# Optimization experiments

Measured on AMD Instinct MI355X. Metric: run time of the kernel, lower is better.

## Reference

```python
import jax, jax.numpy as jnp
import numpy as np

B, C, H, W = 32, 128, 32, 32
E, K, D, HID = 16, 2, 128, 512  # nbExperts, topK, nbIn=nbOut, hidden=4*max(nbIn,nbOut)


def setup_inputs() -> dict:
    key = jax.random.key(0)
    ks = jax.random.split(key, 6)
    init = lambda k, shape, fan: (jax.random.normal(k, shape, jnp.float32) / np.sqrt(fan)).astype(jnp.float32)
    return {
        "x": jax.random.normal(ks[0], (B, C, H, W), jnp.float32),
        "gate_w": init(ks[1], (D, E), D),
        "gate_b": jnp.zeros((E,), jnp.float32),
        "noise_w": init(ks[2], (D, E), D),
        "noise_b": jnp.zeros((E,), jnp.float32),
        "w1": init(ks[3], (E, D, HID), D),
        "b1": jnp.zeros((E, HID), jnp.float32),
        "w2": init(ks[4], (E, HID, D), HID),
        "b2": jnp.zeros((E, D), jnp.float32),
        "top_k": K,
    }


def reference(x, gate_w, gate_b, noise_w, noise_b, w1, b1, w2, b2, top_k):
    b, c, h, w = x.shape
    xt = x.transpose(0, 2, 3, 1).reshape(-1, c)  # [T, D] tokens (fromCNN path)
    T = xt.shape[0]

    # --- GatingWithNoise: gate(x) + randn * softplus(noise(x)) ---
    logits = xt @ gate_w + gate_b                      # [T, E]
    noise_sd = jax.nn.softplus(xt @ noise_w + noise_b)  # [T, E]
    noise = jax.random.normal(jax.random.key(42), logits.shape, logits.dtype)
    logits = logits + noise * noise_sd

    # --- top-k, softmax over k, scatter to dense [T, E] gate matrix ---
    top_vals, top_idx = jax.lax.top_k(logits, top_k)   # [T, K]
    probs = jax.nn.softmax(top_vals, axis=1)           # [T, K]
    gates = jnp.zeros((T, E), x.dtype).at[jnp.arange(T)[:, None], top_idx].set(probs)

    # --- dense path: run every expert, weighted combine ---
    hdn = jax.nn.relu(jnp.einsum('td,edh->teh', xt, w1) + b1)  # [T, E, HID]
    eo = jnp.einsum('teh,ehd->ted', hdn, w2) + b2              # [T, E, D]
    out = jnp.einsum('te,ted->td', gates, eo)                  # [T, D]

    out = out.reshape(b, h, w, c).transpose(0, 3, 1, 2)        # back to NCHW
    gates = gates.reshape(b, h, w, E)
    return out, gates
```

## Files before the change

### kernel.cpp

```cpp
#include <hip/hip_runtime.h>
#include <stdint.h>

#define NB       32
#define NC       128
#define NHW      1024
#define NT       32768
#define NE       16
#define NHID     512

typedef __attribute__((ext_vector_type(8))) short short8v;
typedef __attribute__((ext_vector_type(4))) float f32x4;

__device__ __forceinline__ unsigned short f2bf(float f) {
    uint32_t u = __float_as_uint(f);
    uint32_t r = u + 0x7fffu + ((u >> 16) & 1u);
    return (unsigned short)(r >> 16);
}
__device__ __forceinline__ float bf2f(unsigned short u) {
    return __uint_as_float(((uint32_t)u) << 16);
}

__device__ __forceinline__ void gll16(const void* g, void* l) {
    __builtin_amdgcn_global_load_lds(
        (const __attribute__((address_space(1))) uint32_t*)g,
        (__attribute__((address_space(3))) uint32_t*)l, 16, 0, 0);
}

#define WAIT_VMLGKM() asm volatile("s_waitcnt vmcnt(0) lgkmcnt(0)" ::: "memory")
#define WAIT_LGKM()   asm volatile("s_waitcnt lgkmcnt(0)" ::: "memory")
#define SBAR()        { asm volatile("" ::: "memory"); __builtin_amdgcn_s_barrier(); asm volatile("" ::: "memory"); }

__device__ __forceinline__ uint32_t rotl32(uint32_t x, uint32_t d) {
    return (x << d) | (x >> (32u - d));
}

__device__ __forceinline__ void threefry2x32_20(uint32_t k0, uint32_t k1,
                                                uint32_t& x0, uint32_t& x1) {
    const uint32_t ks0 = k0, ks1 = k1, ks2 = k0 ^ k1 ^ 0x1BD11BDAu;
    x0 += ks0; x1 += ks1;
#define TFR(r) { x0 += x1; x1 = rotl32(x1, r); x1 ^= x0; }
    TFR(13u) TFR(15u) TFR(26u) TFR(6u)
    x0 += ks1; x1 += ks2 + 1u;
    TFR(17u) TFR(29u) TFR(16u) TFR(24u)
    x0 += ks2; x1 += ks0 + 2u;
    TFR(13u) TFR(15u) TFR(26u) TFR(6u)
    x0 += ks0; x1 += ks1 + 3u;
    TFR(17u) TFR(29u) TFR(16u) TFR(24u)
    x0 += ks1; x1 += ks2 + 4u;
    TFR(13u) TFR(15u) TFR(26u) TFR(6u)
    x0 += ks2; x1 += ks0 + 5u;
#undef TFR
}

__device__ __forceinline__ float erfinv_xla_f32(float x) {
    float w = -log1pf(-x * x);
    float p;
    if (w < 5.0f) {
        w = w - 2.5f;
        p = 2.81022636e-08f;
        p = fmaf(p, w, 3.43273939e-07f);
        p = fmaf(p, w, -3.5233877e-06f);
        p = fmaf(p, w, -4.39150654e-06f);
        p = fmaf(p, w, 0.00021858087f);
        p = fmaf(p, w, -0.00125372503f);
        p = fmaf(p, w, -0.00417768164f);
        p = fmaf(p, w, 0.246640727f);
        p = fmaf(p, w, 1.50140941f);
    } else {
        w = sqrtf(w) - 3.0f;
        p = -0.000200214257f;
        p = fmaf(p, w, 0.000100950558f);
        p = fmaf(p, w, 0.00134934322f);
        p = fmaf(p, w, -0.00367342844f);
        p = fmaf(p, w, 0.00573950773f);
        p = fmaf(p, w, -0.0076224613f);
        p = fmaf(p, w, 0.00943887047f);
        p = fmaf(p, w, 1.00167406f);
        p = fmaf(p, w, 2.83297682f);
    }
    return p * x;
}

__device__ __forceinline__ float jax_noise_elem(uint32_t i) {
    uint32_t x0 = 0u, x1 = i;
    threefry2x32_20(0u, 42u, x0, x1);
    uint32_t bits = x0 ^ x1;
    float f = __uint_as_float(0x3f800000u | (bits >> 9)) - 1.0f;
    const float lo = -0.99999994f;
    float u = f * 2.0f + lo;
    u = fmaxf(lo, u);
    return 1.41421354f * erfinv_xla_f32(u);
}

__global__ __launch_bounds__(256) void moe_gate_kernel(
    const float* __restrict__ x,
    const float* __restrict__ gate_w, const float* __restrict__ gate_b,
    const float* __restrict__ noise_w, const float* __restrict__ noise_b,
    float* __restrict__ gates_out,
    int*   __restrict__ top_idx,
    float* __restrict__ top_prob,
    int*   __restrict__ rank,
    int*   __restrict__ cnt,
    unsigned short* __restrict__ xtb,
    int do_new)
{
    __shared__ float lw[32 * 160];
    __shared__ int   lcnt[16];
    __shared__ int   lbase[16];

    const int tid = threadIdx.x;
    const int tl  = tid >> 2;
    const int q   = tid & 3;
    const int t   = blockIdx.x * 64 + tl;
    const int b   = t >> 10, hw = t & 1023;

    if (tid < 16) lcnt[tid] = 0;

    for (int idx = tid; idx < 4096; idx += 256) {
        int ci = idx >> 7;
        int r  = idx & 127;
        int qq = r >> 5, e = r & 31;
        int c  = qq * 32 + ci;
        float v = (e < 16) ? gate_w[c * 16 + e] : noise_w[c * 16 + (e - 16)];
        lw[ci * 160 + qq * 40 + e] = v;
    }
    __syncthreads();

    float acc[32];
    #pragma unroll
    for (int e = 0; e < 32; ++e) acc[e] = 0.f;

    unsigned short xh[32];
    const float* xq = x + (size_t)b * (NC * NHW) + (size_t)(q * 32) * NHW + hw;
    const float* wq = lw + q * 40;
    #pragma unroll 4
    for (int ci = 0; ci < 32; ++ci) {
        float xv = xq[(size_t)ci << 10];
        xh[ci] = f2bf(xv);
        const f32x4* wr = (const f32x4*)(wq + ci * 160);
        #pragma unroll
        for (int j = 0; j < 8; ++j) {
            f32x4 w4 = wr[j];
            #pragma unroll
            for (int k = 0; k < 4; ++k)
                acc[j * 4 + k] = fmaf(xv, w4[k], acc[j * 4 + k]);
        }
    }

    if (do_new) {
        #pragma unroll
        for (int j = 0; j < 4; ++j) {
            short8v v;
            #pragma unroll
            for (int k = 0; k < 8; ++k) v[k] = (short)xh[j * 8 + k];
            *(short8v*)(xtb + (size_t)t * 128 + q * 32 + j * 8) = v;
        }
    }

    #pragma unroll
    for (int e = 0; e < 32; ++e) {
        acc[e] += __shfl_xor(acc[e], 1);
        acc[e] += __shfl_xor(acc[e], 2);
    }

    float lg[4];
    #pragma unroll
    for (int j = 0; j < 4; ++j) {
        int e = q * 4 + j;
        float g  = acc[e] + gate_b[e];
        float an = acc[16 + e] + noise_b[e];
        float sd = fmaxf(an, 0.f) + log1pf(expf(-fabsf(an)));
        float nz = jax_noise_elem((uint32_t)t * 16u + (uint32_t)e);
        lg[j] = fmaf(nz, sd, g);
    }

    float v1 = lg[0], v2 = -INFINITY;
    int   i1 = q * 4, i2 = 0x7fffffff;
    #pragma unroll
    for (int j = 1; j < 4; ++j) {
        float v = lg[j]; int e = q * 4 + j;
        if (v > v1) { v2 = v1; i2 = i1; v1 = v; i1 = e; }
        else if (v > v2) { v2 = v; i2 = e; }
    }
    #pragma unroll
    for (int m = 1; m <= 2; m <<= 1) {
        float pv1 = __shfl_xor(v1, m), pv2 = __shfl_xor(v2, m);
        int   pi1 = __shfl_xor(i1, m), pi2 = __shfl_xor(i2, m);
        bool pBest = (pv1 > v1) || (pv1 == v1 && pi1 < i1);
        float c2v; int c2i;
        if (pBest) { c2v = v1;  c2i = i1;  v1 = pv1; i1 = pi1;
                     if (!((c2v > pv2) || (c2v == pv2 && c2i < pi2))) { c2v = pv2; c2i = pi2; }
        } else     { c2v = pv1; c2i = pi1;
                     if (!((c2v > v2)  || (c2v == v2  && c2i < i2)))  { c2v = v2;  c2i = i2;  }
        }
        v2 = c2v; i2 = c2i;
    }

    float qq = expf(v2 - v1);
    float s  = 1.0f + qq;
    float p1 = 1.0f / s;
    float p2 = qq / s;

    f32x4 g4;
    #pragma unroll
    for (int j = 0; j < 4; ++j) {
        int e = q * 4 + j;
        g4[j] = (e == i1) ? p1 : ((e == i2) ? p2 : 0.f);
    }
    *(f32x4*)(gates_out + (size_t)t * 16 + q * 4) = g4;

    int r1 = 0, r2 = 0;
    if (q == 0) {
        top_idx[t * 2 + 0] = i1;  top_idx[t * 2 + 1] = i2;
        top_prob[t * 2 + 0] = p1; top_prob[t * 2 + 1] = p2;
        if (do_new) {
            r1 = atomicAdd(&lcnt[i1], 1);
            r2 = atomicAdd(&lcnt[i2], 1);
        }
    }
    if (do_new) {
        __syncthreads();
        if (tid < 16) lbase[tid] = atomicAdd(&cnt[tid], lcnt[tid]);
        __syncthreads();
        if (q == 0) {
            rank[t * 2 + 0] = lbase[i1] + r1;
            rank[t * 2 + 1] = lbase[i2] + r2;
        }
    }
}

__global__ __launch_bounds__(256) void transpose_convert_kernel(
    const float* __restrict__ src, unsigned short* __restrict__ dst, int R, int C)
{
    __shared__ float ts[64][65];
    const int nr = R >> 6, ncc = C >> 6;
    const int blk = blockIdx.x;
    const int e = blk / (nr * ncc);
    const int rem = blk % (nr * ncc);
    const int rt = rem / ncc, ct = rem % ncc;
    const float* S = src + (size_t)e * R * C + (size_t)(rt * 64) * C + ct * 64;
    unsigned short* D = dst + (size_t)e * R * C + (size_t)(ct * 64) * R + rt * 64;
    const int tid = threadIdx.x;
    #pragma unroll
    for (int i = 0; i < 16; ++i) {
        int lin = i * 256 + tid;
        int r = lin >> 6, c = lin & 63;
        ts[r][c] = S[(size_t)r * C + c];
    }
    __syncthreads();
    #pragma unroll
    for (int i = 0; i < 16; ++i) {
        int lin = i * 256 + tid;
        int c = lin >> 6, r = lin & 63;
        D[(size_t)c * R + r] = f2bf(ts[r][c]);
    }
}

__global__ __launch_bounds__(256) void scan_kernel(
    const int* __restrict__ cnt,
    int* __restrict__ poff, int* __restrict__ blk2e,
    int* __restrict__ blk2chunk, int* __restrict__ total_chunks,
    int* __restrict__ pair_tok)
{
    __shared__ int snch[16];
    __shared__ int scum[17];
    __shared__ int spoff[16];
    const int tid = threadIdx.x;
    if (tid < 16) snch[tid] = (cnt[tid] + 127) >> 7;
    __syncthreads();
    if (tid == 0) {
        int cc = 0, off = 0;
        for (int e = 0; e < 16; ++e) {
            scum[e] = cc; spoff[e] = off;
            cc += snch[e]; off += snch[e] << 7;
        }
        scum[16] = cc;
        *total_chunks = cc;
    }
    __syncthreads();
    const int tot = scum[16];
    for (int idx = tid; idx < tot; idx += 256) {
        int e = 0;
        #pragma unroll
        for (int k = 0; k < 15; ++k)
            if (idx >= scum[k + 1]) e = k + 1;
        blk2e[idx] = e;
        blk2chunk[idx] = idx - scum[e];
    }
    if (tid < 16) poff[tid] = spoff[tid];
    for (int e = 0; e < 16; ++e) {
        int start = spoff[e] + cnt[e];
        int end   = spoff[e] + (snch[e] << 7);
        for (int i = start + tid; i < end; i += 256)
            pair_tok[i] = -1;
    }
}

__global__ __launch_bounds__(256) void scatter_kernel(
    const int* __restrict__ top_idx, const int* __restrict__ rank,
    const int* __restrict__ poff, int* __restrict__ pair_tok,
    int* __restrict__ slot_of)
{
    int i = blockIdx.x * 256 + threadIdx.x;
    int t = i >> 1;
    int e = top_idx[i];
    int slot = poff[e] + rank[i];
    pair_tok[slot] = t;
    slot_of[i] = slot;
}

__device__ __forceinline__ void stage_w1(const unsigned short* w1e, short* W1s,
                                         int hcn, int wid, int lane) {
    #pragma unroll
    for (int k2 = 0; k2 < 2; ++k2) {
        int i2 = wid * 2 + k2;
        int r2 = i2 * 4 + (lane >> 4);
        int s2 = lane & 15;
        gll16(w1e + (size_t)(hcn + r2) * 128 + ((s2 ^ (r2 & 15)) * 8),
              W1s + i2 * 512);
    }
}
__device__ __forceinline__ void stage_w2(const unsigned short* w2e, short* W2s,
                                         int hcn, int wid, int lane) {
    #pragma unroll
    for (int k2 = 0; k2 < 2; ++k2) {
        int i2 = wid * 2 + k2;
        int r2 = i2 * 8 + (lane >> 3);
        int s2 = lane & 7;
        gll16(w2e + (size_t)r2 * 512 + hcn + ((s2 ^ (r2 & 7)) * 8),
              W2s + i2 * 512);
    }
}

__global__ __launch_bounds__(512, 4) void moe_mfma_kernel(
    const unsigned short* __restrict__ xtb,
    const int* __restrict__ pair_tok, const int* __restrict__ blk2e,
    const int* __restrict__ blk2chunk, const int* __restrict__ poff,
    const int* __restrict__ total_chunks,
    const unsigned short* __restrict__ w1bt,
    const float* __restrict__ b1,
    const unsigned short* __restrict__ w2bt,
    const float* __restrict__ b2,
    unsigned short* __restrict__ pair_y)
{
    __shared__ short Xs[128 * 128];
    __shared__ short Hs[128 * 64];
    __shared__ short W1s[64 * 128];
    __shared__ short W2s[128 * 64];

    const int blk = blockIdx.x;
    if (blk >= *total_chunks) return;
    const int e  = blk2e[blk];
    const int p0 = poff[e] + (blk2chunk[blk] << 7);
    const int tid  = threadIdx.x;
    const int lane = tid & 63;
    const int wid  = tid >> 6;
    const int wm   = wid >> 1;
    const int wn   = wid & 1;
    const int l16  = lane & 15;
    const int lg   = lane >> 4;

    const unsigned short* w1e = w1bt + (size_t)e * 512 * 128;
    const unsigned short* w2e = w2bt + (size_t)e * 128 * 512;

    stage_w1(w1e, W1s, 0, wid, lane);
    stage_w2(w2e, W2s, 0, wid, lane);

    #pragma unroll
    for (int i = 0; i < 4; ++i) {
        int lin = i * 512 + tid;
        int row = lin >> 4, kc = lin & 15;
        int tok = pair_tok[p0 + row];
        short8v v = {};
        if (tok >= 0)
            v = *(const short8v*)(xtb + (size_t)tok * 128 + kc * 8);
        *(short8v*)(Xs + row * 128 + ((kc ^ (row & 15)) * 8)) = v;
    }

    f32x4 yacc[2][4];
    #pragma unroll
    for (int mi = 0; mi < 2; ++mi)
        #pragma unroll
        for (int ni = 0; ni < 4; ++ni)
            yacc[mi][ni] = (f32x4){0.f, 0.f, 0.f, 0.f};

    const int rowA0 = wm * 32 + l16, rowA1 = rowA0 + 16;

    for (int c = 0; c < 8; ++c) {
        WAIT_VMLGKM(); SBAR();

        f32x4 hacc[2][2];
        #pragma unroll
        for (int mi = 0; mi < 2; ++mi)
            #pragma unroll
            for (int ni = 0; ni < 2; ++ni)
                hacc[mi][ni] = (f32x4){0.f, 0.f, 0.f, 0.f};

        #pragma unroll
        for (int kk = 0; kk < 4; ++kk) {
            int slot = kk * 4 + lg;
            short8v a0 = *(const short8v*)(Xs + rowA0 * 128 + ((slot ^ (rowA0 & 15)) * 8));
            short8v a1 = *(const short8v*)(Xs + rowA1 * 128 + ((slot ^ (rowA1 & 15)) * 8));
            #pragma unroll
            for (int ni = 0; ni < 2; ++ni) {
                int hr = wn * 32 + ni * 16 + l16;
                short8v bfr = *(const short8v*)(W1s + hr * 128 + ((slot ^ (hr & 15)) * 8));
                hacc[0][ni] = __builtin_amdgcn_mfma_f32_16x16x32_bf16(a0, bfr, hacc[0][ni], 0, 0, 0);
                hacc[1][ni] = __builtin_amdgcn_mfma_f32_16x16x32_bf16(a1, bfr, hacc[1][ni], 0, 0, 0);
            }
        }
        #pragma unroll
        for (int ni = 0; ni < 2; ++ni) {
            int col = wn * 32 + ni * 16 + l16;
            float b1v = b1[e * 512 + (c << 6) + col];
            #pragma unroll
            for (int mi = 0; mi < 2; ++mi) {
                #pragma unroll
                for (int r = 0; r < 4; ++r) {
                    int m = wm * 32 + mi * 16 + lg * 4 + r;
                    float v = fmaxf(hacc[mi][ni][r] + b1v, 0.f);
                    Hs[m * 64 + (((col >> 3) ^ (m & 7)) << 3) + (col & 7)] = (short)f2bf(v);
                }
            }
        }
        WAIT_LGKM(); SBAR();

        if (c < 7) stage_w1(w1e, W1s, (c + 1) << 6, wid, lane);

        #pragma unroll
        for (int kk = 0; kk < 2; ++kk) {
            int slot = kk * 4 + lg;
            short8v a0 = *(const short8v*)(Hs + rowA0 * 64 + ((slot ^ (rowA0 & 7)) * 8));
            short8v a1 = *(const short8v*)(Hs + rowA1 * 64 + ((slot ^ (rowA1 & 7)) * 8));
            #pragma unroll
            for (int ni = 0; ni < 4; ++ni) {
                int dr = wn * 64 + ni * 16 + l16;
                short8v bfr = *(const short8v*)(W2s + dr * 64 + ((slot ^ (dr & 7)) * 8));
                yacc[0][ni] = __builtin_amdgcn_mfma_f32_16x16x32_bf16(a0, bfr, yacc[0][ni], 0, 0, 0);
                yacc[1][ni] = __builtin_amdgcn_mfma_f32_16x16x32_bf16(a1, bfr, yacc[1][ni], 0, 0, 0);
            }
        }
        WAIT_LGKM(); SBAR();

        if (c < 7) stage_w2(w2e, W2s, (c + 1) << 6, wid, lane);
    }

    #pragma unroll
    for (int ni = 0; ni < 4; ++ni) {
        int d = wn * 64 + ni * 16 + l16;
        float b2v = b2[e * 128 + d];
        #pragma unroll
        for (int mi = 0; mi < 2; ++mi) {
            #pragma unroll
            for (int r = 0; r < 4; ++r) {
                int m = wm * 32 + mi * 16 + lg * 4 + r;
                pair_y[(size_t)(p0 + m) * 128 + d] = f2bf(yacc[mi][ni][r] + b2v);
            }
        }
    }
}

__global__ __launch_bounds__(256) void combine_kernel(
    const unsigned short* __restrict__ pair_y, const int* __restrict__ slot_of,
    const float* __restrict__ top_prob, float* __restrict__ out)
{
    __shared__ float ob[64][129];
    const int blk = blockIdx.x;
    const int b = blk >> 4;
    const int hw0 = (blk & 15) << 6;
    const int tid = threadIdx.x;
    #pragma unroll
    for (int i = 0; i < 4; ++i) {
        int lin = i * 256 + tid;
        int tl = lin >> 4, dg = lin & 15;
        int t = b * 1024 + hw0 + tl;
        int s0 = slot_of[t * 2], s1 = slot_of[t * 2 + 1];
        float p0 = top_prob[t * 2], p1 = top_prob[t * 2 + 1];
        short8v y0 = *(const short8v*)(pair_y + (size_t)s0 * 128 + dg * 8);
        short8v y1 = *(const short8v*)(pair_y + (size_t)s1 * 128 + dg * 8);
        #pragma unroll
        for (int j = 0; j < 8; ++j)
            ob[tl][dg * 8 + j] = p0 * bf2f((unsigned short)y0[j]) + p1 * bf2f((unsigned short)y1[j]);
    }
    __syncthreads();
    #pragma unroll
    for (int i = 0; i < 32; ++i) {
        int lin = i * 256 + tid;
        int d = lin >> 6, hwl = lin & 63;
        out[((size_t)b * 128 + d) * 1024 + hw0 + hwl] = ob[hwl][d];
    }
}

__global__ __launch_bounds__(256) void moe_expert_kernel(
    const float* __restrict__ x,
    const int* __restrict__ top_idx, const float* __restrict__ top_prob,
    const float* __restrict__ w1, const float* __restrict__ b1,
    const float* __restrict__ w2, const float* __restrict__ b2,
    float* __restrict__ out)
{
    __shared__ float xsB[128];
    __shared__ float hb[512];

    const int tid = threadIdx.x;
    const int t = blockIdx.x;
    const int b = t >> 10, hw = t & 1023;

    if (tid < 128)
        xsB[tid] = x[((size_t)b * 128 + tid) * NHW + hw];
    __syncthreads();

    float oacc = 0.f;
    #pragma unroll
    for (int k = 0; k < 2; ++k) {
        const int e = top_idx[t * 2 + k];
        const float pw = top_prob[t * 2 + k];
        const float* W1 = w1 + (size_t)e * (128 * 512);
        float a0 = 0.f, a1 = 0.f;
        for (int d = 0; d < 128; ++d) {
            float xv = xsB[d];
            a0 = fmaf(xv, W1[d * 512 + tid], a0);
            a1 = fmaf(xv, W1[d * 512 + tid + 256], a1);
        }
        hb[tid]       = fmaxf(a0 + b1[e * 512 + tid], 0.f);
        hb[tid + 256] = fmaxf(a1 + b1[e * 512 + tid + 256], 0.f);
        __syncthreads();
        if (tid < 128) {
            const float* W2 = w2 + (size_t)e * (512 * 128);
            float a = 0.f;
            for (int h = 0; h < 512; ++h)
                a = fmaf(hb[h], W2[h * 128 + tid], a);
            oacc = fmaf(pw, a + b2[e * 128 + tid], oacc);
        }
        __syncthreads();
    }
    if (tid < 128)
        out[((size_t)b * 128 + tid) * NHW + hw] = oacc;
}

extern "C" void kernel_launch(void* const* d_in, const int* in_sizes, int n_in,
                              void* d_out, int out_size, void* d_ws, size_t ws_size,
                              hipStream_t stream) {
    const float* x       = (const float*)d_in[0];
    const float* gate_w  = (const float*)d_in[1];
    const float* gate_b  = (const float*)d_in[2];
    const float* noise_w = (const float*)d_in[3];
    const float* noise_b = (const float*)d_in[4];
    const float* w1      = (const float*)d_in[5];
    const float* b1      = (const float*)d_in[6];
    const float* w2      = (const float*)d_in[7];
    const float* b2      = (const float*)d_in[8];

    float* out   = (float*)d_out;
    float* gates = out + (size_t)NB * NC * NHW;

    const size_t OFF_CNT    = 0;
    const size_t OFF_POFF   = 1024;
    const size_t OFF_TOTAL  = 2048;
    const size_t OFF_B2E    = 4096;
    const size_t OFF_B2C    = 8192;
    const size_t OFF_TIDX   = 12288;
    const size_t OFF_RANK   = OFF_TIDX + (size_t)NT * 2 * 4;
    const size_t OFF_SLOT   = OFF_RANK + (size_t)NT * 2 * 4;
    const size_t OFF_PROB   = OFF_SLOT + (size_t)NT * 2 * 4;
    const size_t OFF_XTB    = OFF_PROB + (size_t)NT * 2 * 4;
    const size_t OFF_W1BT   = OFF_XTB + (size_t)NT * 128 * 2;
    const size_t OFF_W2BT   = OFF_W1BT + (size_t)NE * 512 * 128 * 2;
    const size_t OFF_PTOK   = OFF_W2BT + (size_t)NE * 128 * 512 * 2;
    const size_t NPAIR_PAD  = 67584;
    const size_t OFF_PAIRY  = OFF_PTOK + NPAIR_PAD * 4;
    const size_t NEED       = OFF_PAIRY + NPAIR_PAD * 128 * 2;

    char* ws = (char*)d_ws;
    int*   cnt      = (int*)(ws + OFF_CNT);
    int*   poff     = (int*)(ws + OFF_POFF);
    int*   total_ch = (int*)(ws + OFF_TOTAL);
    int*   blk2e    = (int*)(ws + OFF_B2E);
    int*   blk2c    = (int*)(ws + OFF_B2C);
    int*   top_idx  = (int*)(ws + OFF_TIDX);
    int*   rank     = (int*)(ws + OFF_RANK);
    int*   slot_of  = (int*)(ws + OFF_SLOT);
    float* top_prob = (float*)(ws + OFF_PROB);
    unsigned short* xtb    = (unsigned short*)(ws + OFF_XTB);
    unsigned short* w1bt   = (unsigned short*)(ws + OFF_W1BT);
    unsigned short* w2bt   = (unsigned short*)(ws + OFF_W2BT);
    int*   pair_tok = (int*)(ws + OFF_PTOK);
    unsigned short* pair_y = (unsigned short*)(ws + OFF_PAIRY);

    const int use_new = (ws_size >= NEED) ? 1 : 0;

    if (use_new)
        hipMemsetAsync(cnt, 0, 16 * sizeof(int), stream);

    moe_gate_kernel<<<NT / 64, 256, 0, stream>>>(
        x, gate_w, gate_b, noise_w, noise_b,
        gates, top_idx, top_prob, rank, cnt, xtb, use_new);

    if (use_new) {
        transpose_convert_kernel<<<NE * 2 * 8, 256, 0, stream>>>(w1, w1bt, 128, 512);
        transpose_convert_kernel<<<NE * 8 * 2, 256, 0, stream>>>(w2, w2bt, 512, 128);
        scan_kernel<<<1, 256, 0, stream>>>(cnt, poff, blk2e, blk2c, total_ch, pair_tok);
        scatter_kernel<<<NT * 2 / 256, 256, 0, stream>>>(top_idx, rank, poff, pair_tok, slot_of);
        moe_mfma_kernel<<<528, 512, 0, stream>>>(
            xtb, pair_tok, blk2e, blk2c, poff, total_ch,
            w1bt, b1, w2bt, b2, pair_y);
        combine_kernel<<<512, 256, 0, stream>>>(pair_y, slot_of, top_prob, out);
    } else {
        moe_expert_kernel<<<NT, 256, 0, stream>>>(
            x, top_idx, top_prob, w1, b1, w2, b2, out);
    }
}
```

Baseline: 96.68 us.

## Replace global atomic expert counters with per-block counts and merge transpose launches

The gate kernel now writes per-block expert counts and local ranks instead of doing global atomicAdd on shared counters. The scan kernel computes per-block base offsets with a two-level prefix sum, and scatter uses those bases. This removes the memset launch and the global atomics, and makes slot assignment deterministic. The two weight transpose launches are also merged into one, cutting launch overhead. In exchange the single-block scan kernel does more serial work.

Measured after the change: 95.64 us. No clear change (-1.1%).

```diff
diff --git a/kernel.cpp b/kernel.cpp
--- a/kernel.cpp
+++ b/kernel.cpp
@@ -7,6 +7,7 @@
 #define NT       32768
 #define NE       16
 #define NHID     512
+#define NGBLK    512
 
 typedef __attribute__((ext_vector_type(8))) short short8v;
 typedef __attribute__((ext_vector_type(4))) float f32x4;
@@ -100,13 +101,12 @@
     int*   __restrict__ top_idx,
     float* __restrict__ top_prob,
     int*   __restrict__ rank,
-    int*   __restrict__ cnt,
+    int*   __restrict__ bcnt,
     unsigned short* __restrict__ xtb,
     int do_new)
 {
     __shared__ float lw[32 * 160];
     __shared__ int   lcnt[16];
-    __shared__ int   lbase[16];
 
     const int tid = threadIdx.x;
     const int tl  = tid >> 2;
@@ -209,32 +209,32 @@
     }
     *(f32x4*)(gates_out + (size_t)t * 16 + q * 4) = g4;
 
-    int r1 = 0, r2 = 0;
     if (q == 0) {
         top_idx[t * 2 + 0] = i1;  top_idx[t * 2 + 1] = i2;
         top_prob[t * 2 + 0] = p1; top_prob[t * 2 + 1] = p2;
         if (do_new) {
-            r1 = atomicAdd(&lcnt[i1], 1);
-            r2 = atomicAdd(&lcnt[i2], 1);
+            int r1 = atomicAdd(&lcnt[i1], 1);
+            int r2 = atomicAdd(&lcnt[i2], 1);
+            rank[t * 2 + 0] = r1;
+            rank[t * 2 + 1] = r2;
         }
     }
     if (do_new) {
         __syncthreads();
-        if (tid < 16) lbase[tid] = atomicAdd(&cnt[tid], lcnt[tid]);
-        __syncthreads();
-        if (q == 0) {
-            rank[t * 2 + 0] = lbase[i1] + r1;
-            rank[t * 2 + 1] = lbase[i2] + r2;
-        }
-    }
-}
-
-__global__ __launch_bounds__(256) void transpose_convert_kernel(
-    const float* __restrict__ src, unsigned short* __restrict__ dst, int R, int C)
+        if (tid < 16) bcnt[blockIdx.x * 16 + tid] = lcnt[tid];
+    }
+}
+
+__global__ __launch_bounds__(256) void transpose_convert2_kernel(
+    const float* __restrict__ w1, unsigned short* __restrict__ w1bt,
+    const float* __restrict__ w2, unsigned short* __restrict__ w2bt)
 {
     __shared__ float ts[64][65];
+    int blk = blockIdx.x;
+    const float* src;  unsigned short* dst;  int R, C;
+    if (blk < 256) { src = w1; dst = w1bt; R = 128; C = 512; }
+    else           { src = w2; dst = w2bt; R = 512; C = 128; blk -= 256; }
     const int nr = R >> 6, ncc = C >> 6;
-    const int blk = blockIdx.x;
     const int e = blk / (nr * ncc);
     const int rem = blk % (nr * ncc);
     const int rt = rem / ncc, ct = rem % ncc;
@@ -257,22 +257,40 @@
 }
 
 __global__ __launch_bounds__(256) void scan_kernel(
-    const int* __restrict__ cnt,
+    const int* __restrict__ bcnt,
     int* __restrict__ poff, int* __restrict__ blk2e,
     int* __restrict__ blk2chunk, int* __restrict__ total_chunks,
+    int* __restrict__ bbase,
     int* __restrict__ pair_tok)
 {
+    __shared__ int ps[16][17];
+    __shared__ int gb[16][17];
+    __shared__ int scnt[16];
     __shared__ int snch[16];
     __shared__ int scum[17];
     __shared__ int spoff[16];
     const int tid = threadIdx.x;
-    if (tid < 16) snch[tid] = (cnt[tid] + 127) >> 7;
+    const int e = tid >> 4, g = tid & 15;
+
+    int s = 0;
+    for (int b = g * 32; b < g * 32 + 32; ++b)
+        s += bcnt[b * 16 + e];
+    ps[e][g] = s;
     __syncthreads();
+
+    if (tid < 16) {
+        int run = 0;
+        for (int gg = 0; gg < 16; ++gg) { gb[tid][gg] = run; run += ps[tid][gg]; }
+        scnt[tid] = run;
+        snch[tid] = (run + 127) >> 7;
+    }
+    __syncthreads();
+
     if (tid == 0) {
         int cc = 0, off = 0;
-        for (int e = 0; e < 16; ++e) {
-            scum[e] = cc; spoff[e] = off;
-            cc += snch[e]; off += snch[e] << 7;
+        for (int ee = 0; ee < 16; ++ee) {
+            scum[ee] = cc; spoff[ee] = off;
+            cc += snch[ee]; off += snch[ee] << 7;
         }
         scum[16] = cc;
         *total_chunks = cc;
@@ -280,17 +298,26 @@
     __syncthreads();
     const int tot = scum[16];
     for (int idx = tid; idx < tot; idx += 256) {
-        int e = 0;
+        int ee = 0;
         #pragma unroll
         for (int k = 0; k < 15; ++k)
-            if (idx >= scum[k + 1]) e = k + 1;
-        blk2e[idx] = e;
-        blk2chunk[idx] = idx - scum[e];
+            if (idx >= scum[k + 1]) ee = k + 1;
+        blk2e[idx] = ee;
+        blk2chunk[idx] = idx - scum[ee];
     }
     if (tid < 16) poff[tid] = spoff[tid];
-    for (int e = 0; e < 16; ++e) {
-        int start = spoff[e] + cnt[e];
-        int end   = spoff[e] + (snch[e] << 7);
+
+    {
+        int run = spoff[e] + gb[e][g];
+        for (int b = g * 32; b < g * 32 + 32; ++b) {
+            bbase[b * 16 + e] = run;
+            run += bcnt[b * 16 + e];
+        }
+    }
+
+    for (int ee = 0; ee < 16; ++ee) {
+        int start = spoff[ee] + scnt[ee];
+        int end   = spoff[ee] + (snch[ee] << 7);
         for (int i = start + tid; i < end; i += 256)
             pair_tok[i] = -1;
     }
@@ -298,13 +325,13 @@
 
 __global__ __launch_bounds__(256) void scatter_kernel(
     const int* __restrict__ top_idx, const int* __restrict__ rank,
-    const int* __restrict__ poff, int* __restrict__ pair_tok,
+    const int* __restrict__ bbase, int* __restrict__ pair_tok,
     int* __restrict__ slot_of)
 {
     int i = blockIdx.x * 256 + threadIdx.x;
     int t = i >> 1;
     int e = top_idx[i];
-    int slot = poff[e] + rank[i];
+    int slot = bbase[(t >> 6) * 16 + e] + rank[i];
     pair_tok[slot] = t;
     slot_of[i] = slot;
 }
@@ -553,25 +580,25 @@
     float* out   = (float*)d_out;
     float* gates = out + (size_t)NB * NC * NHW;
 
-    const size_t OFF_CNT    = 0;
-    const size_t OFF_POFF   = 1024;
-    const size_t OFF_TOTAL  = 2048;
+    const size_t OFF_POFF   = 0;
+    const size_t OFF_TOTAL  = 1024;
     const size_t OFF_B2E    = 4096;
     const size_t OFF_B2C    = 8192;
     const size_t OFF_TIDX   = 12288;
-    const size_t OFF_RANK   = OFF_TIDX + (size_t)NT * 2 * 4;
-    const size_t OFF_SLOT   = OFF_RANK + (size_t)NT * 2 * 4;
-    const size_t OFF_PROB   = OFF_SLOT + (size_t)NT * 2 * 4;
-    const size_t OFF_XTB    = OFF_PROB + (size_t)NT * 2 * 4;
-    const size_t OFF_W1BT   = OFF_XTB + (size_t)NT * 128 * 2;
-    const size_t OFF_W2BT   = OFF_W1BT + (size_t)NE * 512 * 128 * 2;
-    const size_t OFF_PTOK   = OFF_W2BT + (size_t)NE * 128 * 512 * 2;
+    const size_t OFF_RANK   = OFF_TIDX  + (size_t)NT * 2 * 4;
+    const size_t OFF_SLOT   = OFF_RANK  + (size_t)NT * 2 * 4;
+    const size_t OFF_PROB   = OFF_SLOT  + (size_t)NT * 2 * 4;
+    const size_t OFF_BCNT   = OFF_PROB  + (size_t)NT * 2 * 4;
+    const size_t OFF_BBASE  = OFF_BCNT  + (size_t)NGBLK * 16 * 4;
+    const size_t OFF_XTB    = OFF_BBASE + (size_t)NGBLK * 16 * 4;
+    const size_t OFF_W1BT   = OFF_XTB   + (size_t)NT * 128 * 2;
+    const size_t OFF_W2BT   = OFF_W1BT  + (size_t)NE * 512 * 128 * 2;
+    const size_t OFF_PTOK   = OFF_W2BT  + (size_t)NE * 128 * 512 * 2;
     const size_t NPAIR_PAD  = 67584;
-    const size_t OFF_PAIRY  = OFF_PTOK + NPAIR_PAD * 4;
+    const size_t OFF_PAIRY  = OFF_PTOK  + NPAIR_PAD * 4;
     const size_t NEED       = OFF_PAIRY + NPAIR_PAD * 128 * 2;
 
     char* ws = (char*)d_ws;
-    int*   cnt      = (int*)(ws + OFF_CNT);
     int*   poff     = (int*)(ws + OFF_POFF);
     int*   total_ch = (int*)(ws + OFF_TOTAL);
     int*   blk2e    = (int*)(ws + OFF_B2E);
@@ -580,6 +607,8 @@
     int*   rank     = (int*)(ws + OFF_RANK);
     int*   slot_of  = (int*)(ws + OFF_SLOT);
     float* top_prob = (float*)(ws + OFF_PROB);
+    int*   bcnt     = (int*)(ws + OFF_BCNT);
+    int*   bbase    = (int*)(ws + OFF_BBASE);
     unsigned short* xtb    = (unsigned short*)(ws + OFF_XTB);
     unsigned short* w1bt   = (unsigned short*)(ws + OFF_W1BT);
     unsigned short* w2bt   = (unsigned short*)(ws + OFF_W2BT);
@@ -588,18 +617,16 @@
 
     const int use_new = (ws_size >= NEED) ? 1 : 0;
 
-    if (use_new)
-        hipMemsetAsync(cnt, 0, 16 * sizeof(int), stream);
-
     moe_gate_kernel<<<NT / 64, 256, 0, stream>>>(
         x, gate_w, gate_b, noise_w, noise_b,
-        gates, top_idx, top_prob, rank, cnt, xtb, use_new);
+        gates, top_idx, top_prob, rank, bcnt, xtb, use_new);
 
     if (use_new) {
-        transpose_convert_kernel<<<NE * 2 * 8, 256, 0, stream>>>(w1, w1bt, 128, 512);
-        transpose_convert_kernel<<<NE * 8 * 2, 256, 0, stream>>>(w2, w2bt, 512, 128);
-        scan_kernel<<<1, 256, 0, stream>>>(cnt, poff, blk2e, blk2c, total_ch, pair_tok);
-        scatter_kernel<<<NT * 2 / 256, 256, 0, stream>>>(top_idx, rank, poff, pair_tok, slot_of);
+        transpose_convert2_kernel<<<512, 256, 0, stream>>>(w1, w1bt, w2, w2bt);
+        scan_kernel<<<1, 256, 0, stream>>>(bcnt, poff, blk2e, blk2c, total_ch,
+                                           bbase, pair_tok);
+        scatter_kernel<<<NT * 2 / 256, 256, 0, stream>>>(top_idx, rank, bbase,
+                                                         pair_tok, slot_of);
         moe_mfma_kernel<<<528, 512, 0, stream>>>(
             xtb, pair_tok, blk2e, blk2c, poff, total_ch,
             w1bt, b1, w2bt, b2, pair_y);
```
